# Kernel optimization log

Measured on AMD Instinct MI355X. Metric: run time of the kernel, lower is better.

## Reference

```python
import jax, jax.numpy as jnp
import numpy as np

C, B, N, L = 4, 8, 4096, 1024


def setup_inputs() -> dict:
    key = jax.random.key(0)
    inputs = jax.random.normal(key, (C, B, N, L), dtype=jnp.float32)
    return {"inputs": inputs}


def reference(inputs) -> jnp.ndarray:
    # Original: for each [N, L] box_input, divide each row elementwise by
    # range(1..L) and reduce_sum over the last axis. Vectorized across all
    # leading dims via broadcasting. Output shape [C, B, N].
    L_ = inputs.shape[-1]
    probability_numbers = jnp.arange(1, L_ + 1, dtype=inputs.dtype)  # [L]
    return jnp.sum(inputs / probability_numbers, axis=-1)
```

## Files before the change

kernel.cpp:

```cpp
#include <hip/hip_runtime.h>


constexpr int kL = 1024;

__global__ __launch_bounds__(256) void FractalDimension_kernel(
    const float* __restrict__ in, float* __restrict__ out) {
  const int row = blockIdx.x;
  const int tid = threadIdx.x;

  const float4* p = reinterpret_cast<const float4*>(in + (size_t)row * kL);
  float4 v = p[tid];

  const float b0 = (float)(4 * tid + 1);
  float s = v.x / b0 + v.y / (b0 + 1.0f) + v.z / (b0 + 2.0f) + v.w / (b0 + 3.0f);

  #pragma unroll
  for (int off = 32; off > 0; off >>= 1)
    s += __shfl_down(s, off, 64);

  __shared__ float partial[4];
  const int wave = tid >> 6;
  if ((tid & 63) == 0) partial[wave] = s;
  __syncthreads();

  if (tid == 0)
    out[row] = (partial[0] + partial[1]) + (partial[2] + partial[3]);
}

extern "C" void kernel_launch(void* const* d_in, const int* in_sizes, int n_in,
                              void* d_out, int out_size, void* d_ws, size_t ws_size,
                              hipStream_t stream) {
  const float* in = (const float*)d_in[0];
  float* out = (float*)d_out;
  const int rows = in_sizes[0] / kL;
  FractalDimension_kernel<<<rows, 256, 0, stream>>>(in, out);
}
```

Baseline: 649.1 us.

## Use persistent wave-per-row grid-stride kernel with precomputed reciprocals and FMAs

Replaces the one-block-per-row launch with a fixed grid where each 64-lane wave reduces two rows per iteration in a grid-stride loop. Reciprocals of 1..L are precomputed in registers so per-element divides become FMAs, and the shared-memory cross-wave reduction and barrier are removed. This aims to increase bytes in flight per thread and cut launch/block scheduling and divide overhead. It adds register pressure for the 16 reciprocals and a fixed grid size that may not match occupancy ideally.

```diff
diff --git a/kernel.cpp b/kernel.cpp
--- a/kernel.cpp
+++ b/kernel.cpp
@@ -4,34 +4,61 @@
 constexpr int kL = 1024;
 
 __global__ __launch_bounds__(256) void FractalDimension_kernel(
-    const float* __restrict__ in, float* __restrict__ out) {
-  const int row = blockIdx.x;
-  const int tid = threadIdx.x;
+    const float* __restrict__ in, float* __restrict__ out, int rows) {
+  const int lane = threadIdx.x & 63;
+  const int gwave = (int)((blockIdx.x * blockDim.x + threadIdx.x) >> 6);
+  const int nwaves = (int)((gridDim.x * blockDim.x) >> 6);
 
-  const float4* p = reinterpret_cast<const float4*>(in + (size_t)row * kL);
-  float4 v = p[tid];
+  float r[4][4];
+#pragma unroll
+  for (int it = 0; it < 4; ++it) {
+#pragma unroll
+    for (int j = 0; j < 4; ++j) {
+      r[it][j] = 1.0f / (float)(it * 256 + lane * 4 + j + 1);
+    }
+  }
 
-  const float b0 = (float)(4 * tid + 1);
-  float s = v.x / b0 + v.y / (b0 + 1.0f) + v.z / (b0 + 2.0f) + v.w / (b0 + 3.0f);
+  for (int row = gwave * 2; row < rows; row += 2 * nwaves) {
+    const bool has2 = (row + 1) < rows;
+    const float4* p0 =
+        reinterpret_cast<const float4*>(in + (size_t)row * kL) + lane;
+    const float4* p1 = p0 + (kL / 4);
 
-  #pragma unroll
-  for (int off = 32; off > 0; off >>= 1)
-    s += __shfl_down(s, off, 64);
+    float s0 = 0.0f, s1 = 0.0f;
+#pragma unroll
+    for (int it = 0; it < 4; ++it) {
+      float4 v0 = p0[it * 64];
+      s0 = fmaf(v0.x, r[it][0], s0);
+      s0 = fmaf(v0.y, r[it][1], s0);
+      s0 = fmaf(v0.z, r[it][2], s0);
+      s0 = fmaf(v0.w, r[it][3], s0);
+      if (has2) {
+        float4 v1 = p1[it * 64];
+        s1 = fmaf(v1.x, r[it][0], s1);
+        s1 = fmaf(v1.y, r[it][1], s1);
+        s1 = fmaf(v1.z, r[it][2], s1);
+        s1 = fmaf(v1.w, r[it][3], s1);
+      }
+    }
 
-  __shared__ float partial[4];
-  const int wave = tid >> 6;
-  if ((tid & 63) == 0) partial[wave] = s;
-  __syncthreads();
+#pragma unroll
+    for (int off = 32; off > 0; off >>= 1) {
+      s0 += __shfl_down(s0, off, 64);
+      s1 += __shfl_down(s1, off, 64);
+    }
 
-  if (tid == 0)
-    out[row] = (partial[0] + partial[1]) + (partial[2] + partial[3]);
+    if (lane == 0) {
+      out[row] = s0;
+      if (has2) out[row + 1] = s1;
+    }
+  }
 }
 
 extern "C" void kernel_launch(void* const* d_in, const int* in_sizes, int n_in,
-                              void* d_out, int out_size, void* d_ws, size_t ws_size,
-                              hipStream_t stream) {
+                              void* d_out, int out_size, void* d_ws,
+                              size_t ws_size, hipStream_t stream) {
   const float* in = (const float*)d_in[0];
   float* out = (float*)d_out;
   const int rows = in_sizes[0] / kL;
-  FractalDimension_kernel<<<rows, 256, 0, stream>>>(in, out);
+  FractalDimension_kernel<<<2048, 256, 0, stream>>>(in, out, rows);
 }
```

New measurement: 670.8 us. +3.3%, slower.

## Use persistent wave-per-row loop with precomputed reciprocals and nontemporal loads

Applied to the files above, without the earlier changes.

Replaces the block-per-row launch with a fixed grid where each wave processes whole rows in a grid-stride loop. Each lane issues four vector loads per row and multiplies by reciprocals computed once per lane instead of dividing per element. This removes the shared-memory reduction and barrier. The aim is more memory-level parallelism and lower launch and ALU overhead, at the cost of slightly different rounding from reciprocal multiplication.

```diff
diff --git a/kernel.cpp b/kernel.cpp
--- a/kernel.cpp
+++ b/kernel.cpp
@@ -3,35 +3,60 @@
 
 constexpr int kL = 1024;
 
+typedef float f32x4 __attribute__((ext_vector_type(4)));
+
 __global__ __launch_bounds__(256) void FractalDimension_kernel(
-    const float* __restrict__ in, float* __restrict__ out) {
-  const int row = blockIdx.x;
-  const int tid = threadIdx.x;
+    const float* __restrict__ in, float* __restrict__ out, int rows) {
+  const int lane = threadIdx.x & 63;
+  const int gwave = (int)((blockIdx.x * blockDim.x + threadIdx.x) >> 6);
+  const int nwaves = (int)((gridDim.x * blockDim.x) >> 6);
 
-  const float4* p = reinterpret_cast<const float4*>(in + (size_t)row * kL);
-  float4 v = p[tid];
+  const float b = (float)(lane * 4 + 1);
+  const float r00 = 1.0f / (b + 0.0f),   r01 = 1.0f / (b + 1.0f);
+  const float r02 = 1.0f / (b + 2.0f),   r03 = 1.0f / (b + 3.0f);
+  const float r10 = 1.0f / (b + 256.0f), r11 = 1.0f / (b + 257.0f);
+  const float r12 = 1.0f / (b + 258.0f), r13 = 1.0f / (b + 259.0f);
+  const float r20 = 1.0f / (b + 512.0f), r21 = 1.0f / (b + 513.0f);
+  const float r22 = 1.0f / (b + 514.0f), r23 = 1.0f / (b + 515.0f);
+  const float r30 = 1.0f / (b + 768.0f), r31 = 1.0f / (b + 769.0f);
+  const float r32 = 1.0f / (b + 770.0f), r33 = 1.0f / (b + 771.0f);
 
-  const float b0 = (float)(4 * tid + 1);
-  float s = v.x / b0 + v.y / (b0 + 1.0f) + v.z / (b0 + 2.0f) + v.w / (b0 + 3.0f);
+  for (int row = gwave; row < rows; row += nwaves) {
+    const f32x4* p =
+        reinterpret_cast<const f32x4*>(in + (size_t)row * kL) + lane;
 
-  #pragma unroll
-  for (int off = 32; off > 0; off >>= 1)
-    s += __shfl_down(s, off, 64);
+    f32x4 v0 = __builtin_nontemporal_load(p);
+    f32x4 v1 = __builtin_nontemporal_load(p + 64);
+    f32x4 v2 = __builtin_nontemporal_load(p + 128);
+    f32x4 v3 = __builtin_nontemporal_load(p + 192);
 
-  __shared__ float partial[4];
-  const int wave = tid >> 6;
-  if ((tid & 63) == 0) partial[wave] = s;
-  __syncthreads();
+    float a0 = v0.x * r00, a1 = v1.x * r10, a2 = v2.x * r20, a3 = v3.x * r30;
+    a0 = fmaf(v0.y, r01, a0);
+    a1 = fmaf(v1.y, r11, a1);
+    a2 = fmaf(v2.y, r21, a2);
+    a3 = fmaf(v3.y, r31, a3);
+    a0 = fmaf(v0.z, r02, a0);
+    a1 = fmaf(v1.z, r12, a1);
+    a2 = fmaf(v2.z, r22, a2);
+    a3 = fmaf(v3.z, r32, a3);
+    a0 = fmaf(v0.w, r03, a0);
+    a1 = fmaf(v1.w, r13, a1);
+    a2 = fmaf(v2.w, r23, a2);
+    a3 = fmaf(v3.w, r33, a3);
+    float s = (a0 + a1) + (a2 + a3);
 
-  if (tid == 0)
-    out[row] = (partial[0] + partial[1]) + (partial[2] + partial[3]);
+#pragma unroll
+    for (int off = 32; off > 0; off >>= 1) s += __shfl_down(s, off, 64);
+
+    if (lane == 0) out[row] = s;
+  }
 }
 
 extern "C" void kernel_launch(void* const* d_in, const int* in_sizes, int n_in,
-                              void* d_out, int out_size, void* d_ws, size_t ws_size,
-                              hipStream_t stream) {
+                              void* d_out, int out_size, void* d_ws,
+                              size_t ws_size, hipStream_t stream) {
   const float* in = (const float*)d_in[0];
   float* out = (float*)d_out;
   const int rows = in_sizes[0] / kL;
-  FractalDimension_kernel<<<rows, 256, 0, stream>>>(in, out);
+  FractalDimension_kernel<<<2048, 256, 0, stream>>>(in, out, rows);
 }
```

Measured after the change: 652.5 us. Within noise of the previous version (+0.5%).
